# Kernel optimization log

Hardware: AMD Instinct MI355X
Metric: run time of the kernel (lower is better)

Reference implementation:

```python
import jax, jax.numpy as jnp
import numpy as np
from jax import lax

B, S, F, H, NH = 64, 128, 16, 64, 2
STATIC, OUT = 32, 2
FC_IN = 2 * F * H + 32 + 8  # 2088


def setup_inputs() -> dict:
    key = jax.random.key(0)
    ks = iter(jax.random.split(key, 40))
    def n(shp, s=0.05):
        return (jax.random.normal(next(ks), shp) * s).astype(jnp.float32)
    inp = {
        "workday_input": n((B, S, F), 1.0),
        "restday_input": n((B, S, F), 1.0),
        "static_input": n((B, STATIC), 1.0),
        "time_gap": n((B, 1), 1.0),
        # per-feature LSTMs (input_size=1) stacked over feature axis F
        "wd_Wih": n((F, 4 * H)), "wd_Whh": n((F, 4 * H, H)),
        "wd_bih": n((F, 4 * H)), "wd_bhh": n((F, 4 * H)),
        "rd_Wih": n((F, 4 * H)), "rd_Whh": n((F, 4 * H, H)),
        "rd_bih": n((F, 4 * H)), "rd_bhh": n((F, 4 * H)),
        # per-feature MultiheadAttention params stacked over F
        "wd_attn_w": n((F, 3 * H, H)), "wd_attn_b": n((F, 3 * H)),
        "wd_out_w": n((F, H, H)), "wd_out_b": n((F, H)),
        "rd_attn_w": n((F, 3 * H, H)), "rd_attn_b": n((F, 3 * H)),
        "rd_out_w": n((F, H, H)), "rd_out_b": n((F, H)),
        # dnn for static features
        "d1_w": n((64, STATIC)), "d1_b": n((64,)),
        "d2_w": n((32, 64)), "d2_b": n((32,)),
        # time-aware module
        "t1_w": n((16, 1)), "t1_b": n((16,)),
        "t2_w": n((8, 16)), "t2_b": n((8,)),
        # final fc
        "fc_w": n((OUT, FC_IN)), "fc_b": n((OUT,)),
    }
    return inp


def _lstm(x, Wih, Whh, bih, bhh):
    # x: [B,S,F], Wih: [F,4H] (input dim 1 squeezed), Whh: [F,4H,H]
    b = (bih + bhh)[None]  # [1,F,4H]
    def step(carry, x_t):
        h, c = carry  # [B,F,H]
        gates = x_t[:, :, None] * Wih[None] + jnp.einsum('bfh,fgh->bfg', h, Whh) + b
        i, f, g, o = jnp.split(gates, 4, axis=-1)
        i, f, o = jax.nn.sigmoid(i), jax.nn.sigmoid(f), jax.nn.sigmoid(o)
        c = f * c + i * jnp.tanh(g)
        h = o * jnp.tanh(c)
        return (h, c), h
    h0 = jnp.zeros((x.shape[0], x.shape[2], Whh.shape[-1]), x.dtype)
    _, hs = lax.scan(step, (h0, h0), jnp.moveaxis(x, 1, 0))  # [S,B,F,H]
    return jnp.moveaxis(hs, 0, 1)  # [B,S,F,H]


def _mha(x, Win, bin_, Wout, bout):
    # x: [B,F,S,H]; torch MultiheadAttention, num_heads=NH, avg attn weights
    hd = H // NH
    qkv = jnp.einsum('bfsh,fgh->bfsg', x, Win) + bin_[None, :, None, :]
    q, k, v = jnp.split(qkv, 3, axis=-1)  # each [B,F,S,H]
    def heads(t):  # [B,F,S,H] -> [B,F,NH,S,hd]
        return jnp.moveaxis(t.reshape(t.shape[:3] + (NH, hd)), 3, 2)
    q, k, v = heads(q), heads(k), heads(v)
    scores = jnp.einsum('bfnqd,bfnkd->bfnqk', q, k) / jnp.sqrt(jnp.asarray(hd, x.dtype))
    w = jax.nn.softmax(scores, axis=-1)  # [B,F,NH,S,S]
    o = jnp.einsum('bfnqk,bfnkd->bfnqd', w, v)
    o = jnp.moveaxis(o, 2, 3).reshape(x.shape)  # [B,F,S,H]
    o = jnp.einsum('bfsh,foh->bfso', o, Wout) + bout[None, :, None, :]
    return o, w.mean(axis=2)  # out [B,F,S,H], attn [B,F,S,S]


def _branch(x, Wih, Whh, bih, bhh, Win, bin_, Wout, bout):
    lstm_out = jnp.moveaxis(_lstm(x, Wih, Whh, bih, bhh), 1, 2)  # [B,F,S,H]
    attn_out, attn_w = _mha(lstm_out, Win, bin_, Wout, bout)
    pooled = attn_out.mean(axis=2)  # [B,F,H] (mean over seq)
    return pooled, attn_w


def reference(workday_input, restday_input, static_input, time_gap,
              wd_Wih, wd_Whh, wd_bih, wd_bhh, rd_Wih, rd_Whh, rd_bih, rd_bhh,
              wd_attn_w, wd_attn_b, wd_out_w, wd_out_b,
              rd_attn_w, rd_attn_b, rd_out_w, rd_out_b,
              d1_w, d1_b, d2_w, d2_b, t1_w, t1_b, t2_w, t2_b, fc_w, fc_b):
    wd_pooled, wd_attn = _branch(workday_input, wd_Wih, wd_Whh, wd_bih, wd_bhh,
                                 wd_attn_w, wd_attn_b, wd_out_w, wd_out_b)
    rd_pooled, rd_attn = _branch(restday_input, rd_Wih, rd_Whh, rd_bih, rd_bhh,
                                 rd_attn_w, rd_attn_b, rd_out_w, rd_out_b)
    b = workday_input.shape[0]
    combined = jnp.concatenate([wd_pooled.reshape(b, -1), rd_pooled.reshape(b, -1)], axis=1)
    static_f = jax.nn.relu(jax.nn.relu(static_input @ d1_w.T + d1_b) @ d2_w.T + d2_b)
    combined = jnp.concatenate([combined, static_f], axis=1)
    time_f = jax.nn.relu(jax.nn.relu(time_gap @ t1_w.T + t1_b) @ t2_w.T + t2_b)
    combined = jnp.concatenate([combined, time_f], axis=1)
    output = combined @ fc_w.T + fc_b
    # attn weight lists stacked over feature axis: [F,B,S,S]
    return output, jnp.moveaxis(wd_attn, 1, 0), jnp.moveaxis(rd_attn, 1, 0)
```

## Files before the change

kernel.cpp:

```cpp
#include <hip/hip_runtime.h>
#include <hip/hip_bf16.h>

#define BB 64
#define SS 128
#define FF 16
#define HH 64
#define G4 256
#define G3 192

typedef unsigned short ushort_t;
typedef _Float16 f16_t;
typedef f16_t h2 __attribute__((ext_vector_type(2)));
typedef f16_t v8h __attribute__((ext_vector_type(8)));
typedef float v4f __attribute__((ext_vector_type(4)));

static __device__ __forceinline__ float rcpf(float x){
#if __has_builtin(__builtin_amdgcn_rcpf)
    return __builtin_amdgcn_rcpf(x);
#else
    return 1.0f/x;
#endif
}
static __device__ __forceinline__ float sigm(float x){ return rcpf(1.0f + __expf(-x)); }
static __device__ __forceinline__ float tanhfast(float x){ return 2.0f*rcpf(1.0f + __expf(-2.0f*x)) - 1.0f; }
static __device__ __forceinline__ h2 u2h(unsigned u){ return __builtin_bit_cast(h2, u); }
static __device__ __forceinline__ ushort_t f2h(float f){ f16_t h=(f16_t)f; return __builtin_bit_cast(ushort_t, h); }
static __device__ __forceinline__ float h2f(ushort_t u){ return (float)__builtin_bit_cast(f16_t, u); }
static __device__ __forceinline__ h2 mk2(float a, float b){ h2 r; r.x=(f16_t)a; r.y=(f16_t)b; return r; }
static __device__ __forceinline__ float dot2(h2 a, h2 b, float c){
#if __has_builtin(__builtin_amdgcn_fdot2)
    return __builtin_amdgcn_fdot2(a, b, c, false);
#else
    return fmaf((float)a.x,(float)b.x, fmaf((float)a.y,(float)b.y, c));
#endif
}

template<int C>
static __device__ __forceinline__ float dppf(float v){
    return __builtin_bit_cast(float,
        __builtin_amdgcn_update_dpp(0, __builtin_bit_cast(int, v), C, 0xf, 0xf, true));
}
static __device__ __forceinline__ float wred16_max(float v){
    v = fmaxf(v, dppf<0xB1>(v));
    v = fmaxf(v, dppf<0x4E>(v));
    v = fmaxf(v, dppf<0x141>(v));
    v = fmaxf(v, dppf<0x140>(v));
    return v;
}
static __device__ __forceinline__ float wred16_sum(float v){
    v += dppf<0xB1>(v);
    v += dppf<0x4E>(v);
    v += dppf<0x141>(v);
    v += dppf<0x140>(v);
    return v;
}

static __device__ __forceinline__ void ldrow64(const float* p, size_t i, float* w){
    const float4* r = (const float4*)(p + i);
    #pragma unroll
    for (int j=0;j<16;j++){ float4 t=r[j]; w[4*j]=t.x; w[4*j+1]=t.y; w[4*j+2]=t.z; w[4*j+3]=t.w; }
}
static __device__ __forceinline__ v8h cvt8(const float* p){
    float4 a = ((const float4*)p)[0];
    float4 b = ((const float4*)p)[1];
    v8h v;
    v[0]=(f16_t)a.x; v[1]=(f16_t)a.y; v[2]=(f16_t)a.z; v[3]=(f16_t)a.w;
    v[4]=(f16_t)b.x; v[5]=(f16_t)b.y; v[6]=(f16_t)b.z; v[7]=(f16_t)b.w;
    return v;
}

static __device__ __forceinline__ void step_sync(){
    __builtin_amdgcn_sched_barrier(0);
    asm volatile("s_waitcnt lgkmcnt(0)" ::: "memory");
    __builtin_amdgcn_s_barrier();
    __builtin_amdgcn_sched_barrier(0);
}

__global__ void sig_kernel(float* dout, int n, float val){
    int i = blockIdx.x*256 + threadIdx.x;
    if (i < n) dout[i] = val;
}

__global__ __launch_bounds__(64) void init_kernel(
    const float* __restrict__ stat, const float* __restrict__ tg,
    const float* __restrict__ d1w, const float* __restrict__ d1b,
    const float* __restrict__ d2w, const float* __restrict__ d2b,
    const float* __restrict__ t1w, const float* __restrict__ t1b,
    const float* __restrict__ t2w, const float* __restrict__ t2b,
    const float* __restrict__ fcw, const float* __restrict__ fcb,
    float* __restrict__ accb)
{
    const int b = threadIdx.x;
    float sr[32];
    for (int k=0;k<32;++k) sr[k] = stat[(size_t)b*32 + k];
    float h1[64];
    for (int j=0;j<64;++j){
        float a = d1b[j];
        for (int k=0;k<32;++k) a = fmaf(sr[k], d1w[(size_t)j*32+k], a);
        h1[j] = fmaxf(a, 0.0f);
    }
    float sf[32];
    for (int i=0;i<32;++i){
        float a = d2b[i];
        for (int j=0;j<64;++j) a = fmaf(h1[j], d2w[(size_t)i*64+j], a);
        sf[i] = fmaxf(a, 0.0f);
    }
    float tgv = tg[b];
    float th[16];
    for (int j=0;j<16;++j) th[j] = fmaxf(fmaf(tgv, t1w[j], t1b[j]), 0.0f);
    float tf[8];
    for (int i=0;i<8;++i){
        float a = t2b[i];
        for (int j=0;j<16;++j) a = fmaf(th[j], t2w[(size_t)i*16+j], a);
        tf[i] = fmaxf(a, 0.0f);
    }
    float o0 = fcb[0], o1 = fcb[1];
    for (int i=0;i<32;++i){
        o0 = fmaf(sf[i], fcw[2048+i],      o0);
        o1 = fmaf(sf[i], fcw[2088+2048+i], o1);
    }
    for (int i=0;i<8;++i){
        o0 = fmaf(tf[i], fcw[2080+i],      o0);
        o1 = fmaf(tf[i], fcw[2088+2080+i], o1);
    }
    accb[2*b]   = o0;
    accb[2*b+1] = o1;
    if (b == 0) accb[128] = 123.0f;
}

__global__ __launch_bounds__(256) void lstm_kernel(
    const float* __restrict__ wd_x, const float* __restrict__ rd_x,
    const float* __restrict__ wd_Wih, const float* __restrict__ wd_Whh,
    const float* __restrict__ wd_bih, const float* __restrict__ wd_bhh,
    const float* __restrict__ rd_Wih, const float* __restrict__ rd_Whh,
    const float* __restrict__ rd_bih, const float* __restrict__ rd_bhh,
    float* __restrict__ dout)
{
    const int bid = blockIdx.x;
    const int branch = bid >> 6;
    const int f = (bid >> 2) & 15;
    const int q = bid & 3;
    const float* xin = branch ? rd_x   : wd_x;
    const float* Wih = branch ? rd_Wih : wd_Wih;
    const float* Whh = branch ? rd_Whh : wd_Whh;
    const float* bih = branch ? rd_bih : wd_bih;
    const float* bhh = branch ? rd_bhh : wd_bhh;

    __shared__ __align__(16) float xseq[SS][16];
    __shared__ __align__(16) ushort_t stg2[2][16][8][64];

    const int tid  = threadIdx.x;
    const int w    = tid >> 6;
    const int lane = tid & 63;
    const int quad = lane >> 4;
    const int ln   = lane & 15;

    v8h bfr[4][2];
    float wihv[4], bsv[4];
    #pragma unroll
    for (int i=0;i<4;++i){
        const int gate = (w + 4*i)*16 + ln;
        wihv[i] = Wih[f*G4 + gate];
        bsv[i]  = bih[f*G4 + gate] + bhh[f*G4 + gate];
        #pragma unroll
        for (int Ks=0;Ks<2;++Ks){
            const float* wr = Whh + ((size_t)f*G4 + gate)*HH + Ks*32 + quad*8;
            float4 aa = ((const float4*)wr)[0];
            float4 bb = ((const float4*)wr)[1];
            v8h v;
            v[0]=(f16_t)aa.x; v[1]=(f16_t)aa.y; v[2]=(f16_t)aa.z; v[3]=(f16_t)aa.w;
            v[4]=(f16_t)bb.x; v[5]=(f16_t)bb.y; v[6]=(f16_t)bb.z; v[7]=(f16_t)bb.w;
            bfr[i][Ks] = v;
        }
    }
    #pragma unroll
    for (int j=0;j<8;++j){
        int e = tid + 256*j;
        int s = e >> 4, m = e & 15;
        xseq[s][m] = xin[((size_t)(q*16+m)*SS + s)*FF + f];
    }
    {
        #pragma unroll
        for (int jz=0;jz<2;++jz){
            int d = tid + 256*jz;
            int m = d >> 5, c = d & 31;
            *(unsigned*)(&stg2[1][m][7][c*2]) = 0u;
        }
    }
    float c0=0.f, c1=0.f, c2=0.f, c3=0.f;
    __syncthreads();

    ushort_t* const sb = &stg2[0][0][0][0];
    const int physA0 = ((0*4 + quad) ^ (ln & 7)) * 8;
    const int physA1 = ((1*4 + quad) ^ (ln & 7)) * 8;
    const int arow   = ln*512;
    const int hmy  = w*16 + ln;
    const int hblk = hmy >> 3, hlow = hmy & 7;
    int woff[4];
    #pragma unroll
    for (int r=0;r<4;++r){
        const int m = quad*4 + r;
        woff[r] = m*512 + (((hblk ^ (m&7))<<3) | hlow);
    }
    const int cm = tid >> 4, part = tid & 15;
    float* const flbase = dout + 128
        + (size_t)(branch*1024 + f*64 + (q*16 + cm)) * 16384;
    int fsrc[4], fg[4];
    #pragma unroll
    for (int jj=0;jj<4;++jj){
        const int g = part + 16*jj;
        fg[jj]   = g;
        fsrc[jj] = cm*64 + (g>>3)*8 + ((g&7) ^ (cm&7));
    }

    float4 xv = *(const float4*)&xseq[0][quad*4];
    v4f cip[4];
    #pragma unroll
    for (int i=0;i<4;++i){
        v4f ci;
        ci[0] = fmaf(xv.x, wihv[i], bsv[i]);
        ci[1] = fmaf(xv.y, wihv[i], bsv[i]);
        ci[2] = fmaf(xv.z, wihv[i], bsv[i]);
        ci[3] = fmaf(xv.w, wihv[i], bsv[i]);
        cip[i] = ci;
    }

    for (int s=0; s<SS; ++s){
        const int rbuf = ((s+15)>>3) & 1;
        const int rsl  = (s+7) & 7;
        const int wbuf = (s>>3) & 1;
        const ushort_t* ap = sb + rbuf*8192 + arow + rsl*64;
        v8h a0 = *(const v8h*)(ap + physA0);
        v8h a1 = *(const v8h*)(ap + physA1);

        const int sn = (s < SS-1) ? s+1 : s;
        float4 xvn = *(const float4*)&xseq[sn][quad*4];

        v4f acc[4];
        #pragma unroll
        for (int i=0;i<4;++i){
            v4f t = __builtin_amdgcn_mfma_f32_16x16x32_f16(a0, bfr[i][0], cip[i], 0,0,0);
            acc[i] = __builtin_amdgcn_mfma_f32_16x16x32_f16(a1, bfr[i][1], t, 0,0,0);
        }
        #pragma unroll
        for (int i=0;i<4;++i){
            v4f ci;
            ci[0] = fmaf(xvn.x, wihv[i], bsv[i]);
            ci[1] = fmaf(xvn.y, wihv[i], bsv[i]);
            ci[2] = fmaf(xvn.z, wihv[i], bsv[i]);
            ci[3] = fmaf(xvn.w, wihv[i], bsv[i]);
            cip[i] = ci;
        }

        ushort_t* wp = sb + wbuf*8192 + (s&7)*64;
        #pragma unroll
        for (int r=0;r<4;++r){
            float iv = sigm(acc[0][r]);
            float fv = sigm(acc[1][r]);
            float gv = tanhfast(acc[2][r]);
            float ov = sigm(acc[3][r]);
            float& cc = (r==0)?c0:(r==1)?c1:(r==2)?c2:c3;
            cc = fmaf(fv, cc, iv*gv);
            float hv = ov * tanhfast(cc);
            wp[woff[r]] = f2h(hv);
        }
        step_sync();
        if ((s & 7) == 7){
            const uint4* src4 = (const uint4*)(sb + wbuf*8192);
            uint4* dst4 = (uint4*)(flbase + (size_t)(s-7)*32);
            #pragma unroll
            for (int jj=0;jj<4;++jj)
                dst4[fg[jj]] = src4[fsrc[jj]];
        }
    }
}

__global__ __launch_bounds__(256, 3) void attn_kernel(
    const float* __restrict__ wd_aw, const float* __restrict__ wd_ab,
    const float* __restrict__ wd_ow, const float* __restrict__ wd_ob,
    const float* __restrict__ rd_aw, const float* __restrict__ rd_ab,
    const float* __restrict__ rd_ow, const float* __restrict__ rd_ob,
    const float* __restrict__ fcw,
    float* __restrict__ dout, float* __restrict__ accb)
{
    const int bid = blockIdx.x;
    const int branch = bid >> 10;
    const int b = (bid >> 4) & 63;
    const int f = bid & 15;
    const float* aw = branch ? rd_aw : wd_aw;
    const float* ab = branch ? rd_ab : wd_ab;
    const float* ow = branch ? rd_ow : wd_ow;
    const float* ob = branch ? rd_ob : wd_ob;

    const size_t cell = (size_t)branch*1024 + (size_t)f*64 + b;
    float* slot = dout + 128 + cell*16384;

    __shared__ __align__(16) ushort_t xb[SS][64];
    __shared__ __align__(16) ushort_t kb[SS][64];
    __shared__ __align__(16) ushort_t vb[SS][64];
    __shared__ __align__(16) float S[1024];

    float* Sf = S;
    const int tid  = threadIdx.x;
    const int wave = tid >> 6;
    const int lane = tid & 63;
    const int quad = lane >> 4;
    const int ln   = lane & 15;

    {
        const uint4* src = (const uint4*)slot;
        uint4* dst = (uint4*)&xb[0][0];
        #pragma unroll
        for (int j=0;j<4;++j){
            const int g = tid + 256*j;
            const int s = g >> 3, blk = g & 7;
            dst[s*8 + (blk ^ (s&7))] = src[g];
        }
    }
    __syncthreads();

    v8h ax[2][2];
    #pragma unroll
    for (int mt=0;mt<2;++mt){
        const int row = (wave*2+mt)*16 + ln;
        #pragma unroll
        for (int Ks=0;Ks<2;++Ks){
            const int blk = Ks*4 + quad;
            ax[mt][Ks] = *(const v8h*)((const char*)&xb[0][0]
                          + row*128 + ((blk ^ (row&7))<<4));
        }
    }
    const float* awf = aw + (size_t)f*G3*HH;
    const float* abf = ab + (size_t)f*G3;

    #pragma unroll
    for (int nt=0;nt<4;++nt){
        const int g = nt*16 + ln;
        const float* wr = awf + (size_t)(HH + g)*HH + quad*8;
        v8h b0 = cvt8(wr);
        v8h b1 = cvt8(wr + 32);
        const float bias = abf[HH + g];
        #pragma unroll
        for (int mt=0;mt<2;++mt){
            v4f ci; ci[0]=bias; ci[1]=bias; ci[2]=bias; ci[3]=bias;
            ci = __builtin_amdgcn_mfma_f32_16x16x32_f16(ax[mt][0], b0, ci, 0,0,0);
            ci = __builtin_amdgcn_mfma_f32_16x16x32_f16(ax[mt][1], b1, ci, 0,0,0);
            #pragma unroll
            for (int r=0;r<4;++r){
                const int s = (wave*2+mt)*16 + quad*4 + r;
                kb[s][ (((g>>3) ^ (s&7))<<3) | (g&7) ] = f2h(ci[r]);
            }
        }
    }
    #pragma unroll
    for (int nt=0;nt<4;++nt){
        const int g = nt*16 + ln;
        const float* wr = awf + (size_t)(2*HH + g)*HH + quad*8;
        v8h b0 = cvt8(wr);
        v8h b1 = cvt8(wr + 32);
        const float bias = abf[2*HH + g];
        #pragma unroll
        for (int mt=0;mt<2;++mt){
            v4f ci; ci[0]=bias; ci[1]=bias; ci[2]=bias; ci[3]=bias;
            ci = __builtin_amdgcn_mfma_f32_16x16x32_f16(ax[mt][0], b0, ci, 0,0,0);
            ci = __builtin_amdgcn_mfma_f32_16x16x32_f16(ax[mt][1], b1, ci, 0,0,0);
            #pragma unroll
            for (int r=0;r<4;++r){
                const int s = (wave*2+mt)*16 + quad*4 + r;
                vb[s][g] = f2h(ci[r]);
            }
        }
    }
    v4f qacc[2][4];
    #pragma unroll
    for (int nt=0;nt<4;++nt){
        const int g = nt*16 + ln;
        const float* wr = awf + (size_t)g*HH + quad*8;
        v8h b0 = cvt8(wr);
        v8h b1 = cvt8(wr + 32);
        const float bias = abf[g];
        #pragma unroll
        for (int mt=0;mt<2;++mt){
            v4f ci; ci[0]=bias; ci[1]=bias; ci[2]=bias; ci[3]=bias;
            ci = __builtin_amdgcn_mfma_f32_16x16x32_f16(ax[mt][0], b0, ci, 0,0,0);
            qacc[mt][nt] = __builtin_amdgcn_mfma_f32_16x16x32_f16(ax[mt][1], b1, ci, 0,0,0);
        }
    }
    __syncthreads();
    #pragma unroll
    for (int mt=0;mt<2;++mt){
        #pragma unroll
        for (int nt=0;nt<4;++nt){
            #pragma unroll
            for (int r=0;r<4;++r){
                const int s = (wave*2+mt)*16 + quad*4 + r;
                const int g = nt*16 + ln;
                xb[s][ (((g>>3) ^ (s&7))<<3) | (g&7) ] =
                    f2h(qacc[mt][nt][r] * 0.17677669529663687f);
            }
        }
    }
    __syncthreads();

    float cs[8][2];
    #pragma unroll
    for (int i=0;i<8;++i){ cs[i][0]=0.f; cs[i][1]=0.f; }

    #pragma unroll
    for (int mt=0;mt<2;++mt){
        const int mrow = (wave*2+mt)*16;
        v8h aq[2];
        #pragma unroll
        for (int h=0;h<2;++h){
            const int row = mrow + ln;
            const int blk = h*4 + quad;
            aq[h] = *(const v8h*)((const char*)&xb[0][0]
                      + row*128 + ((blk ^ (row&7))<<4));
        }
        v4f sc[8][2];
        #pragma unroll
        for (int nt=0;nt<8;++nt){
            const int trow = nt*16 + ln;
            #pragma unroll
            for (int h=0;h<2;++h){
                const int blk = h*4 + quad;
                v8h bk = *(const v8h*)((const char*)&kb[0][0]
                           + trow*128 + ((blk ^ (trow&7))<<4));
                v4f z; z[0]=0.f; z[1]=0.f; z[2]=0.f; z[3]=0.f;
                sc[nt][h] = __builtin_amdgcn_mfma_f32_16x16x32_f16(aq[h], bk, z, 0,0,0);
            }
        }
        #pragma unroll
        for (int r=0;r<4;++r){
            const int s1 = mrow + quad*4 + r;
            #pragma unroll
            for (int h=0;h<2;++h){
                float m = sc[0][h][r];
                #pragma unroll
                for (int nt=1;nt<8;++nt) m = fmaxf(m, sc[nt][h][r]);
                m = wred16_max(m);
                float e0=__expf(sc[0][h][r]-m), e1=__expf(sc[1][h][r]-m);
                float e2=__expf(sc[2][h][r]-m), e3=__expf(sc[3][h][r]-m);
                float e4=__expf(sc[4][h][r]-m), e5=__expf(sc[5][h][r]-m);
                float e6=__expf(sc[6][h][r]-m), e7=__expf(sc[7][h][r]-m);
                float ssum = ((e0+e1)+(e2+e3)) + ((e4+e5)+(e6+e7));
                ssum = wred16_sum(ssum);
                const float inv = rcpf(ssum);
                sc[0][h][r]=e0*inv; sc[1][h][r]=e1*inv;
                sc[2][h][r]=e2*inv; sc[3][h][r]=e3*inv;
                sc[4][h][r]=e4*inv; sc[5][h][r]=e5*inv;
                sc[6][h][r]=e6*inv; sc[7][h][r]=e7*inv;
                #pragma unroll
                for (int nt=0;nt<8;++nt) cs[nt][h] += sc[nt][h][r];
            }
            #pragma unroll
            for (int nt=0;nt<8;++nt)
                slot[s1*SS + nt*16 + ln] = 0.5f*(sc[nt][0][r] + sc[nt][1][r]);
        }
    }

    #pragma unroll
    for (int nt=0;nt<8;++nt){
        #pragma unroll
        for (int h=0;h<2;++h){
            float v = cs[nt][h];
            v += __shfl_xor(v, 16);
            v += __shfl_xor(v, 32);
            cs[nt][h] = v;
        }
    }
    if (lane < 16){
        #pragma unroll
        for (int nt=0;nt<8;++nt){
            Sf[wave*256 +       nt*16 + lane] = cs[nt][0];
            Sf[wave*256 + 128 + nt*16 + lane] = cs[nt][1];
        }
    }
    __syncthreads();

    {
        float rsum = (Sf[tid] + Sf[256+tid] + Sf[512+tid] + Sf[768+tid]) * (1.0f/128.0f);
        Sf[tid] = rsum;
    }
    __syncthreads();

    {
        const int h = lane;
        const float* rr = &Sf[(h>>5)*128];
        float p0 = 0.0f, p1 = 0.0f;
        const int s2a = wave*32;
        for (int s2=s2a; s2<s2a+32; s2+=2){
            p0 = fmaf(rr[s2],   h2f(vb[s2][h]),   p0);
            p1 = fmaf(rr[s2+1], h2f(vb[s2+1][h]), p1);
        }
        Sf[256 + tid] = p0 + p1;
    }
    __syncthreads();
    if (tid < HH){
        Sf[512+tid] = Sf[256+tid] + Sf[320+tid] + Sf[384+tid] + Sf[448+tid];
    }
    __syncthreads();

    if (tid < HH){
        const int g = tid;
        float w2f[64];
        ldrow64(ow, ((size_t)f*HH + g)*HH, w2f);
        float pacc = ob[f*HH + g];
        const float4* om4 = (const float4*)&Sf[512];
        #pragma unroll
        for (int j=0;j<16;j++){
            float4 o4 = om4[j];
            pacc = fmaf(w2f[4*j+0],o4.x,pacc); pacc = fmaf(w2f[4*j+1],o4.y,pacc);
            pacc = fmaf(w2f[4*j+2],o4.z,pacc); pacc = fmaf(w2f[4*j+3],o4.w,pacc);
        }
        const size_t ci = (size_t)branch*1024 + (size_t)f*64 + g;
        float c0 = pacc * fcw[ci];
        float c1 = pacc * fcw[2088 + ci];
        #pragma unroll
        for (int off=1; off<64; off<<=1){
            c0 += __shfl_xor(c0, off);
            c1 += __shfl_xor(c1, off);
        }
        if (tid == 0){
            atomicAdd(&accb[2*b],   c0);
            atomicAdd(&accb[2*b+1], c1);
        }
    }
}

__global__ __launch_bounds__(64) void fin_kernel(
    const float* __restrict__ accb, float* __restrict__ dout)
{
    const int t = threadIdx.x;
    float v0, v1;
    if (accb[128] != 123.0f){ v0 = 760.0f; v1 = 760.0f; }
    else { v0 = accb[2*t]; v1 = accb[2*t+1]; }
    dout[2*t]   = v0;
    dout[2*t+1] = v1;
}

extern "C" void kernel_launch(void* const* d_in, const int* in_sizes, int n_in,
                              void* d_out, int out_size, void* d_ws, size_t ws_size,
                              hipStream_t stream)
{
    static const int exp_sizes[30] = {
        131072,131072,2048,64,
        4096,262144,4096,4096,  4096,262144,4096,4096,
        196608,3072,65536,1024, 196608,3072,65536,1024,
        2048,64,2048,32, 16,16,128,8, 4176,2 };

    bool ok_sizes = (n_in == 30);
    if (ok_sizes) for (int i=0;i<30;++i) if (in_sizes[i] != exp_sizes[i]) { ok_sizes = false; break; }
    const bool ok_out = (out_size == 33554560);
    const bool ok_ws  = (ws_size >= 1024);

    if (!ok_sizes || !ok_out || !ok_ws){
        float sig = !ok_sizes ? 3000.0f : (!ok_out ? 5000.0f : 7000.0f);
        int n = out_size < 128 ? out_size : 128;
        sig_kernel<<<dim3(1), dim3(256), 0, stream>>>((float*)d_out, n, sig);
        return;
    }

    float* accb = (float*)((char*)d_ws + 64);
    float* out  = (float*)d_out;

    init_kernel<<<dim3(1), dim3(64), 0, stream>>>(
        (const float*)d_in[2], (const float*)d_in[3],
        (const float*)d_in[20], (const float*)d_in[21],
        (const float*)d_in[22], (const float*)d_in[23],
        (const float*)d_in[24], (const float*)d_in[25],
        (const float*)d_in[26], (const float*)d_in[27],
        (const float*)d_in[28], (const float*)d_in[29], accb);

    lstm_kernel<<<dim3(128), dim3(256), 0, stream>>>(
        (const float*)d_in[0], (const float*)d_in[1],
        (const float*)d_in[4], (const float*)d_in[5],
        (const float*)d_in[6], (const float*)d_in[7],
        (const float*)d_in[8], (const float*)d_in[9],
        (const float*)d_in[10], (const float*)d_in[11], out);

    attn_kernel<<<dim3(2048), dim3(256), 0, stream>>>(
        (const float*)d_in[12], (const float*)d_in[13],
        (const float*)d_in[14], (const float*)d_in[15],
        (const float*)d_in[16], (const float*)d_in[17],
        (const float*)d_in[18], (const float*)d_in[19],
        (const float*)d_in[28], out, accb);

    fin_kernel<<<dim3(1), dim3(64), 0, stream>>>(accb, out);
}
```

Baseline: 358.9 us.

## Split attention rows across eight waves and unroll LSTM step loop by eight

The attention kernel now runs 512 threads per block, and each wave handles 16 query rows instead of 32. The column-sum, PV and output reductions are rewritten to combine partials across eight waves. This raises parallelism and cuts per-thread register use, at the cost of extra syncs and reduction passes. Separately, the LSTM time loop is restructured into 16 groups of 8 unrolled steps, which removes the per-step buffer-index arithmetic and the conditional flush.

Result: slower. 399.6 us (+11.3%).

```diff
diff --git a/kernel.cpp b/kernel.cpp
--- a/kernel.cpp
+++ b/kernel.cpp
@@ -26,7 +26,6 @@
 static __device__ __forceinline__ h2 u2h(unsigned u){ return __builtin_bit_cast(h2, u); }
 static __device__ __forceinline__ ushort_t f2h(float f){ f16_t h=(f16_t)f; return __builtin_bit_cast(ushort_t, h); }
 static __device__ __forceinline__ float h2f(ushort_t u){ return (float)__builtin_bit_cast(f16_t, u); }
-static __device__ __forceinline__ h2 mk2(float a, float b){ h2 r; r.x=(f16_t)a; r.y=(f16_t)b; return r; }
 static __device__ __forceinline__ float dot2(h2 a, h2 b, float c){
 #if __has_builtin(__builtin_amdgcn_fdot2)
     return __builtin_amdgcn_fdot2(a, b, c, false);
@@ -225,49 +224,55 @@
         cip[i] = ci;
     }
 
-    for (int s=0; s<SS; ++s){
-        const int rbuf = ((s+15)>>3) & 1;
-        const int rsl  = (s+7) & 7;
-        const int wbuf = (s>>3) & 1;
-        const ushort_t* ap = sb + rbuf*8192 + arow + rsl*64;
-        v8h a0 = *(const v8h*)(ap + physA0);
-        v8h a1 = *(const v8h*)(ap + physA1);
-
-        const int sn = (s < SS-1) ? s+1 : s;
-        float4 xvn = *(const float4*)&xseq[sn][quad*4];
-
-        v4f acc[4];
-        #pragma unroll
-        for (int i=0;i<4;++i){
-            v4f t = __builtin_amdgcn_mfma_f32_16x16x32_f16(a0, bfr[i][0], cip[i], 0,0,0);
-            acc[i] = __builtin_amdgcn_mfma_f32_16x16x32_f16(a1, bfr[i][1], t, 0,0,0);
-        }
-        #pragma unroll
-        for (int i=0;i<4;++i){
-            v4f ci;
-            ci[0] = fmaf(xvn.x, wihv[i], bsv[i]);
-            ci[1] = fmaf(xvn.y, wihv[i], bsv[i]);
-            ci[2] = fmaf(xvn.z, wihv[i], bsv[i]);
-            ci[3] = fmaf(xvn.w, wihv[i], bsv[i]);
-            cip[i] = ci;
-        }
-
-        ushort_t* wp = sb + wbuf*8192 + (s&7)*64;
-        #pragma unroll
-        for (int r=0;r<4;++r){
-            float iv = sigm(acc[0][r]);
-            float fv = sigm(acc[1][r]);
-            float gv = tanhfast(acc[2][r]);
-            float ov = sigm(acc[3][r]);
-            float& cc = (r==0)?c0:(r==1)?c1:(r==2)?c2:c3;
-            cc = fmaf(fv, cc, iv*gv);
-            float hv = ov * tanhfast(cc);
-            wp[woff[r]] = f2h(hv);
-        }
-        step_sync();
-        if ((s & 7) == 7){
-            const uint4* src4 = (const uint4*)(sb + wbuf*8192);
-            uint4* dst4 = (uint4*)(flbase + (size_t)(s-7)*32);
+    #pragma unroll 1
+    for (int g8=0; g8<16; ++g8){
+        const int wb = g8 & 1;
+        ushort_t* const wbp = sb + wb*8192;
+        const ushort_t* const pbp = sb + (wb^1)*8192;
+        #pragma unroll
+        for (int k=0;k<8;++k){
+            const int s = g8*8 + k;
+            const ushort_t* ap = (k==0) ? (pbp + arow + 7*64)
+                                        : (wbp + arow + (k-1)*64);
+            v8h a0 = *(const v8h*)(ap + physA0);
+            v8h a1 = *(const v8h*)(ap + physA1);
+
+            const int sn = (s < SS-1) ? s+1 : s;
+            float4 xvn = *(const float4*)&xseq[sn][quad*4];
+
+            v4f acc[4];
+            #pragma unroll
+            for (int i=0;i<4;++i){
+                v4f t = __builtin_amdgcn_mfma_f32_16x16x32_f16(a0, bfr[i][0], cip[i], 0,0,0);
+                acc[i] = __builtin_amdgcn_mfma_f32_16x16x32_f16(a1, bfr[i][1], t, 0,0,0);
+            }
+            #pragma unroll
+            for (int i=0;i<4;++i){
+                v4f ci;
+                ci[0] = fmaf(xvn.x, wihv[i], bsv[i]);
+                ci[1] = fmaf(xvn.y, wihv[i], bsv[i]);
+                ci[2] = fmaf(xvn.z, wihv[i], bsv[i]);
+                ci[3] = fmaf(xvn.w, wihv[i], bsv[i]);
+                cip[i] = ci;
+            }
+
+            ushort_t* wp = wbp + k*64;
+            #pragma unroll
+            for (int r=0;r<4;++r){
+                float iv = sigm(acc[0][r]);
+                float fv = sigm(acc[1][r]);
+                float gv = tanhfast(acc[2][r]);
+                float ov = sigm(acc[3][r]);
+                float& cc = (r==0)?c0:(r==1)?c1:(r==2)?c2:c3;
+                cc = fmaf(fv, cc, iv*gv);
+                float hv = ov * tanhfast(cc);
+                wp[woff[r]] = f2h(hv);
+            }
+            step_sync();
+        }
+        {
+            const uint4* src4 = (const uint4*)wbp;
+            uint4* dst4 = (uint4*)(flbase + (size_t)(g8*8)*32);
             #pragma unroll
             for (int jj=0;jj<4;++jj)
                 dst4[fg[jj]] = src4[fsrc[jj]];
@@ -275,7 +280,7 @@
     }
 }
 
-__global__ __launch_bounds__(256, 3) void attn_kernel(
+__global__ __launch_bounds__(512, 6) void attn_kernel(
     const float* __restrict__ wd_aw, const float* __restrict__ wd_ab,
     const float* __restrict__ wd_ow, const float* __restrict__ wd_ob,
     const float* __restrict__ rd_aw, const float* __restrict__ rd_ab,
@@ -311,27 +316,27 @@
         const uint4* src = (const uint4*)slot;
         uint4* dst = (uint4*)&xb[0][0];
         #pragma unroll
-        for (int j=0;j<4;++j){
-            const int g = tid + 256*j;
+        for (int j=0;j<2;++j){
+            const int g = tid + 512*j;
             const int s = g >> 3, blk = g & 7;
             dst[s*8 + (blk ^ (s&7))] = src[g];
         }
     }
     __syncthreads();
 
-    v8h ax[2][2];
-    #pragma unroll
-    for (int mt=0;mt<2;++mt){
-        const int row = (wave*2+mt)*16 + ln;
+    v8h ax[2];
+    {
+        const int row = wave*16 + ln;
         #pragma unroll
         for (int Ks=0;Ks<2;++Ks){
             const int blk = Ks*4 + quad;
-            ax[mt][Ks] = *(const v8h*)((const char*)&xb[0][0]
-                          + row*128 + ((blk ^ (row&7))<<4));
+            ax[Ks] = *(const v8h*)((const char*)&xb[0][0]
+                      + row*128 + ((blk ^ (row&7))<<4));
         }
     }
     const float* awf = aw + (size_t)f*G3*HH;
     const float* abf = ab + (size_t)f*G3;
+    const int mrow = wave*16;
 
     #pragma unroll
     for (int nt=0;nt<4;++nt){
@@ -340,16 +345,13 @@
         v8h b0 = cvt8(wr);
         v8h b1 = cvt8(wr + 32);
         const float bias = abf[HH + g];
-        #pragma unroll
-        for (int mt=0;mt<2;++mt){
-            v4f ci; ci[0]=bias; ci[1]=bias; ci[2]=bias; ci[3]=bias;
-            ci = __builtin_amdgcn_mfma_f32_16x16x32_f16(ax[mt][0], b0, ci, 0,0,0);
-            ci = __builtin_amdgcn_mfma_f32_16x16x32_f16(ax[mt][1], b1, ci, 0,0,0);
-            #pragma unroll
-            for (int r=0;r<4;++r){
-                const int s = (wave*2+mt)*16 + quad*4 + r;
-                kb[s][ (((g>>3) ^ (s&7))<<3) | (g&7) ] = f2h(ci[r]);
-            }
+        v4f ci; ci[0]=bias; ci[1]=bias; ci[2]=bias; ci[3]=bias;
+        ci = __builtin_amdgcn_mfma_f32_16x16x32_f16(ax[0], b0, ci, 0,0,0);
+        ci = __builtin_amdgcn_mfma_f32_16x16x32_f16(ax[1], b1, ci, 0,0,0);
+        #pragma unroll
+        for (int r=0;r<4;++r){
+            const int s = mrow + quad*4 + r;
+            kb[s][ (((g>>3) ^ (s&7))<<3) | (g&7) ] = f2h(ci[r]);
         }
     }
     #pragma unroll
@@ -359,19 +361,16 @@
         v8h b0 = cvt8(wr);
         v8h b1 = cvt8(wr + 32);
         const float bias = abf[2*HH + g];
-        #pragma unroll
-        for (int mt=0;mt<2;++mt){
-            v4f ci; ci[0]=bias; ci[1]=bias; ci[2]=bias; ci[3]=bias;
-            ci = __builtin_amdgcn_mfma_f32_16x16x32_f16(ax[mt][0], b0, ci, 0,0,0);
-            ci = __builtin_amdgcn_mfma_f32_16x16x32_f16(ax[mt][1], b1, ci, 0,0,0);
-            #pragma unroll
-            for (int r=0;r<4;++r){
-                const int s = (wave*2+mt)*16 + quad*4 + r;
-                vb[s][g] = f2h(ci[r]);
-            }
-        }
-    }
-    v4f qacc[2][4];
+        v4f ci; ci[0]=bias; ci[1]=bias; ci[2]=bias; ci[3]=bias;
+        ci = __builtin_amdgcn_mfma_f32_16x16x32_f16(ax[0], b0, ci, 0,0,0);
+        ci = __builtin_amdgcn_mfma_f32_16x16x32_f16(ax[1], b1, ci, 0,0,0);
+        #pragma unroll
+        for (int r=0;r<4;++r){
+            const int s = mrow + quad*4 + r;
+            vb[s][g] = f2h(ci[r]);
+        }
+    }
+    v4f qacc[4];
     #pragma unroll
     for (int nt=0;nt<4;++nt){
         const int g = nt*16 + ln;
@@ -379,25 +378,19 @@
         v8h b0 = cvt8(wr);
         v8h b1 = cvt8(wr + 32);
         const float bias = abf[g];
-        #pragma unroll
-        for (int mt=0;mt<2;++mt){
-            v4f ci; ci[0]=bias; ci[1]=bias; ci[2]=bias; ci[3]=bias;
-            ci = __builtin_amdgcn_mfma_f32_16x16x32_f16(ax[mt][0], b0, ci, 0,0,0);
-            qacc[mt][nt] = __builtin_amdgcn_mfma_f32_16x16x32_f16(ax[mt][1], b1, ci, 0,0,0);
-        }
-    }
-    __syncthreads();
-    #pragma unroll
-    for (int mt=0;mt<2;++mt){
-        #pragma unroll
-        for (int nt=0;nt<4;++nt){
-            #pragma unroll
-            for (int r=0;r<4;++r){
-                const int s = (wave*2+mt)*16 + quad*4 + r;
-                const int g = nt*16 + ln;
-                xb[s][ (((g>>3) ^ (s&7))<<3) | (g&7) ] =
-                    f2h(qacc[mt][nt][r] * 0.17677669529663687f);
-            }
+        v4f ci; ci[0]=bias; ci[1]=bias; ci[2]=bias; ci[3]=bias;
+        ci = __builtin_amdgcn_mfma_f32_16x16x32_f16(ax[0], b0, ci, 0,0,0);
+        qacc[nt] = __builtin_amdgcn_mfma_f32_16x16x32_f16(ax[1], b1, ci, 0,0,0);
+    }
+    __syncthreads();
+    #pragma unroll
+    for (int nt=0;nt<4;++nt){
+        #pragma unroll
+        for (int r=0;r<4;++r){
+            const int s = mrow + quad*4 + r;
+            const int g = nt*16 + ln;
+            xb[s][ (((g>>3) ^ (s&7))<<3) | (g&7) ] =
+                f2h(qacc[nt][r] * 0.17677669529663687f);
         }
     }
     __syncthreads();
@@ -406,9 +399,7 @@
     #pragma unroll
     for (int i=0;i<8;++i){ cs[i][0]=0.f; cs[i][1]=0.f; }
 
-    #pragma unroll
-    for (int mt=0;mt<2;++mt){
-        const int mrow = (wave*2+mt)*16;
+    {
         v8h aq[2];
         #pragma unroll
         for (int h=0;h<2;++h){
@@ -469,7 +460,7 @@
             cs[nt][h] = v;
         }
     }
-    if (lane < 16){
+    if (wave < 4 && lane < 16){
         #pragma unroll
         for (int nt=0;nt<8;++nt){
             Sf[wave*256 +       nt*16 + lane] = cs[nt][0];
@@ -477,8 +468,16 @@
         }
     }
     __syncthreads();
-
-    {
+    if (wave >= 4 && lane < 16){
+        #pragma unroll
+        for (int nt=0;nt<8;++nt){
+            Sf[(wave-4)*256 +       nt*16 + lane] += cs[nt][0];
+            Sf[(wave-4)*256 + 128 + nt*16 + lane] += cs[nt][1];
+        }
+    }
+    __syncthreads();
+
+    if (tid < 256){
         float rsum = (Sf[tid] + Sf[256+tid] + Sf[512+tid] + Sf[768+tid]) * (1.0f/128.0f);
         Sf[tid] = rsum;
     }
@@ -488,8 +487,8 @@
         const int h = lane;
         const float* rr = &Sf[(h>>5)*128];
         float p0 = 0.0f, p1 = 0.0f;
-        const int s2a = wave*32;
-        for (int s2=s2a; s2<s2a+32; s2+=2){
+        const int s2a = wave*16;
+        for (int s2=s2a; s2<s2a+16; s2+=2){
             p0 = fmaf(rr[s2],   h2f(vb[s2][h]),   p0);
             p1 = fmaf(rr[s2+1], h2f(vb[s2+1][h]), p1);
         }
@@ -497,7 +496,10 @@
     }
     __syncthreads();
     if (tid < HH){
-        Sf[512+tid] = Sf[256+tid] + Sf[320+tid] + Sf[384+tid] + Sf[448+tid];
+        float o = 0.f;
+        #pragma unroll
+        for (int k=0;k<8;++k) o += Sf[256 + 64*k + tid];
+        Sf[768 + tid] = o;
     }
     __syncthreads();
 
@@ -506,7 +508,7 @@
         float w2f[64];
         ldrow64(ow, ((size_t)f*HH + g)*HH, w2f);
         float pacc = ob[f*HH + g];
-        const float4* om4 = (const float4*)&Sf[512];
+        const float4* om4 = (const float4*)&Sf[768];
         #pragma unroll
         for (int j=0;j<16;j++){
             float4 o4 = om4[j];
@@ -579,7 +581,7 @@
         (const float*)d_in[8], (const float*)d_in[9],
         (const float*)d_in[10], (const float*)d_in[11], out);
 
-    attn_kernel<<<dim3(2048), dim3(256), 0, stream>>>(
+    attn_kernel<<<dim3(2048), dim3(512), 0, stream>>>(
         (const float*)d_in[12], (const float*)d_in[13],
         (const float*)d_in[14], (const float*)d_in[15],
         (const float*)d_in[16], (const float*)d_in[17],
```

## Unroll LSTM steps in groups of eight and keep V in registers

Applied to the files above, without the earlier changes.

The LSTM recurrence loop is restructured into 16 groups of 8 fully unrolled steps, so buffer and slot indices become compile-time constants and the periodic flush no longer needs a runtime branch. In the attention kernel, the V projection now stays in MFMA accumulator registers instead of being written to a shared-memory vb buffer. The probability-weighted V sum is computed from those registers with cross-lane shuffles. This cuts LDS usage and allows launch bounds to rise from 3 to 4 blocks per CU, at the cost of more live registers per thread.

Measured after the change: 366.8 us. 2.2% more time.

```diff
diff --git a/kernel.cpp b/kernel.cpp
--- a/kernel.cpp
+++ b/kernel.cpp
@@ -26,7 +26,6 @@
 static __device__ __forceinline__ h2 u2h(unsigned u){ return __builtin_bit_cast(h2, u); }
 static __device__ __forceinline__ ushort_t f2h(float f){ f16_t h=(f16_t)f; return __builtin_bit_cast(ushort_t, h); }
 static __device__ __forceinline__ float h2f(ushort_t u){ return (float)__builtin_bit_cast(f16_t, u); }
-static __device__ __forceinline__ h2 mk2(float a, float b){ h2 r; r.x=(f16_t)a; r.y=(f16_t)b; return r; }
 static __device__ __forceinline__ float dot2(h2 a, h2 b, float c){
 #if __has_builtin(__builtin_amdgcn_fdot2)
     return __builtin_amdgcn_fdot2(a, b, c, false);
@@ -225,49 +224,55 @@
         cip[i] = ci;
     }
 
-    for (int s=0; s<SS; ++s){
-        const int rbuf = ((s+15)>>3) & 1;
-        const int rsl  = (s+7) & 7;
-        const int wbuf = (s>>3) & 1;
-        const ushort_t* ap = sb + rbuf*8192 + arow + rsl*64;
-        v8h a0 = *(const v8h*)(ap + physA0);
-        v8h a1 = *(const v8h*)(ap + physA1);
-
-        const int sn = (s < SS-1) ? s+1 : s;
-        float4 xvn = *(const float4*)&xseq[sn][quad*4];
-
-        v4f acc[4];
-        #pragma unroll
-        for (int i=0;i<4;++i){
-            v4f t = __builtin_amdgcn_mfma_f32_16x16x32_f16(a0, bfr[i][0], cip[i], 0,0,0);
-            acc[i] = __builtin_amdgcn_mfma_f32_16x16x32_f16(a1, bfr[i][1], t, 0,0,0);
-        }
-        #pragma unroll
-        for (int i=0;i<4;++i){
-            v4f ci;
-            ci[0] = fmaf(xvn.x, wihv[i], bsv[i]);
-            ci[1] = fmaf(xvn.y, wihv[i], bsv[i]);
-            ci[2] = fmaf(xvn.z, wihv[i], bsv[i]);
-            ci[3] = fmaf(xvn.w, wihv[i], bsv[i]);
-            cip[i] = ci;
-        }
-
-        ushort_t* wp = sb + wbuf*8192 + (s&7)*64;
-        #pragma unroll
-        for (int r=0;r<4;++r){
-            float iv = sigm(acc[0][r]);
-            float fv = sigm(acc[1][r]);
-            float gv = tanhfast(acc[2][r]);
-            float ov = sigm(acc[3][r]);
-            float& cc = (r==0)?c0:(r==1)?c1:(r==2)?c2:c3;
-            cc = fmaf(fv, cc, iv*gv);
-            float hv = ov * tanhfast(cc);
-            wp[woff[r]] = f2h(hv);
-        }
-        step_sync();
-        if ((s & 7) == 7){
-            const uint4* src4 = (const uint4*)(sb + wbuf*8192);
-            uint4* dst4 = (uint4*)(flbase + (size_t)(s-7)*32);
+    #pragma unroll 1
+    for (int g8=0; g8<16; ++g8){
+        const int wb = g8 & 1;
+        ushort_t* const wbp = sb + wb*8192;
+        const ushort_t* const pbp = sb + (wb^1)*8192;
+        #pragma unroll
+        for (int k=0;k<8;++k){
+            const int s = g8*8 + k;
+            const ushort_t* ap = (k==0) ? (pbp + arow + 7*64)
+                                        : (wbp + arow + (k-1)*64);
+            v8h a0 = *(const v8h*)(ap + physA0);
+            v8h a1 = *(const v8h*)(ap + physA1);
+
+            const int sn = (s < SS-1) ? s+1 : s;
+            float4 xvn = *(const float4*)&xseq[sn][quad*4];
+
+            v4f acc[4];
+            #pragma unroll
+            for (int i=0;i<4;++i){
+                v4f t = __builtin_amdgcn_mfma_f32_16x16x32_f16(a0, bfr[i][0], cip[i], 0,0,0);
+                acc[i] = __builtin_amdgcn_mfma_f32_16x16x32_f16(a1, bfr[i][1], t, 0,0,0);
+            }
+            #pragma unroll
+            for (int i=0;i<4;++i){
+                v4f ci;
+                ci[0] = fmaf(xvn.x, wihv[i], bsv[i]);
+                ci[1] = fmaf(xvn.y, wihv[i], bsv[i]);
+                ci[2] = fmaf(xvn.z, wihv[i], bsv[i]);
+                ci[3] = fmaf(xvn.w, wihv[i], bsv[i]);
+                cip[i] = ci;
+            }
+
+            ushort_t* wp = wbp + k*64;
+            #pragma unroll
+            for (int r=0;r<4;++r){
+                float iv = sigm(acc[0][r]);
+                float fv = sigm(acc[1][r]);
+                float gv = tanhfast(acc[2][r]);
+                float ov = sigm(acc[3][r]);
+                float& cc = (r==0)?c0:(r==1)?c1:(r==2)?c2:c3;
+                cc = fmaf(fv, cc, iv*gv);
+                float hv = ov * tanhfast(cc);
+                wp[woff[r]] = f2h(hv);
+            }
+            step_sync();
+        }
+        {
+            const uint4* src4 = (const uint4*)wbp;
+            uint4* dst4 = (uint4*)(flbase + (size_t)(g8*8)*32);
             #pragma unroll
             for (int jj=0;jj<4;++jj)
                 dst4[fg[jj]] = src4[fsrc[jj]];
@@ -275,7 +280,7 @@
     }
 }
 
-__global__ __launch_bounds__(256, 3) void attn_kernel(
+__global__ __launch_bounds__(256, 4) void attn_kernel(
     const float* __restrict__ wd_aw, const float* __restrict__ wd_ab,
     const float* __restrict__ wd_ow, const float* __restrict__ wd_ob,
     const float* __restrict__ rd_aw, const float* __restrict__ rd_ab,
@@ -297,7 +302,6 @@
 
     __shared__ __align__(16) ushort_t xb[SS][64];
     __shared__ __align__(16) ushort_t kb[SS][64];
-    __shared__ __align__(16) ushort_t vb[SS][64];
     __shared__ __align__(16) float S[1024];
 
     float* Sf = S;
@@ -352,6 +356,7 @@
             }
         }
     }
+    v4f vacc[2][4];
     #pragma unroll
     for (int nt=0;nt<4;++nt){
         const int g = nt*16 + ln;
@@ -363,12 +368,7 @@
         for (int mt=0;mt<2;++mt){
             v4f ci; ci[0]=bias; ci[1]=bias; ci[2]=bias; ci[3]=bias;
             ci = __builtin_amdgcn_mfma_f32_16x16x32_f16(ax[mt][0], b0, ci, 0,0,0);
-            ci = __builtin_amdgcn_mfma_f32_16x16x32_f16(ax[mt][1], b1, ci, 0,0,0);
-            #pragma unroll
-            for (int r=0;r<4;++r){
-                const int s = (wave*2+mt)*16 + quad*4 + r;
-                vb[s][g] = f2h(ci[r]);
-            }
+            vacc[mt][nt] = __builtin_amdgcn_mfma_f32_16x16x32_f16(ax[mt][1], b1, ci, 0,0,0);
         }
     }
     v4f qacc[2][4];
@@ -485,15 +485,27 @@
     __syncthreads();
 
     {
-        const int h = lane;
-        const float* rr = &Sf[(h>>5)*128];
-        float p0 = 0.0f, p1 = 0.0f;
-        const int s2a = wave*32;
-        for (int s2=s2a; s2<s2a+32; s2+=2){
-            p0 = fmaf(rr[s2],   h2f(vb[s2][h]),   p0);
-            p1 = fmaf(rr[s2+1], h2f(vb[s2+1][h]), p1);
-        }
-        Sf[256 + tid] = p0 + p1;
+        float part[4];
+        #pragma unroll
+        for (int nt=0;nt<4;++nt){
+            const float* rr = &Sf[(nt>>1)*128];
+            float p = 0.f;
+            #pragma unroll
+            for (int mt=0;mt<2;++mt){
+                const int t0 = (wave*2+mt)*16 + quad*4;
+                #pragma unroll
+                for (int r=0;r<4;++r)
+                    p = fmaf(rr[t0+r], vacc[mt][nt][r], p);
+            }
+            p += __shfl_xor(p, 16);
+            p += __shfl_xor(p, 32);
+            part[nt] = p;
+        }
+        if (lane < 16){
+            #pragma unroll
+            for (int nt=0;nt<4;++nt)
+                Sf[256 + wave*64 + nt*16 + lane] = part[nt];
+        }
     }
     __syncthreads();
     if (tid < HH){
```
